# Kernel optimization log

Measured on AMD Instinct MI355X. Metric: run time of the kernel, lower is better.

## Reference

```python
import jax, jax.numpy as jnp
import numpy as np

NUM_TAG = 1024
TAG_DIM = 128
COMMITMENT_COST = 0.25
B, W = 128, 1024


def setup_inputs() -> dict:
    key = jax.random.key(0)
    k1, k2 = jax.random.split(key)
    inputs = jax.random.normal(k1, (B, W, TAG_DIM), dtype=jnp.float32)
    # torch init: uniform_(-1/num_tag, 1/num_tag)
    codebook = jax.random.uniform(k2, (NUM_TAG, TAG_DIM), dtype=jnp.float32,
                                  minval=-1.0 / NUM_TAG, maxval=1.0 / NUM_TAG)
    return {"inputs": inputs, "codebook": codebook}


def reference(inputs, codebook):
    # inputs: [B, W, D], codebook: [K, D]
    D = inputs.shape[-1]
    flat = inputs.reshape(-1, D)  # [N, D]
    distances = (jnp.sum(flat * flat, axis=1, keepdims=True)
                 + jnp.sum(codebook * codebook, axis=1)
                 - 2.0 * flat @ codebook.T)
    encoding_indices = jnp.argmin(distances, axis=1)  # [N]
    quantized = codebook[encoding_indices].reshape(inputs.shape)  # [B, W, D]
    e_latent_loss = jnp.mean((jax.lax.stop_gradient(quantized) - inputs) ** 2)
    q_latent_loss = jnp.mean((quantized - jax.lax.stop_gradient(inputs)) ** 2)
    vq_loss = q_latent_loss + COMMITMENT_COST * e_latent_loss
    # straight-through estimator
    quantized_st = inputs + jax.lax.stop_gradient(quantized - inputs)
    return (quantized_st, vq_loss, encoding_indices.reshape(inputs.shape[:-1]))
```

## Files before the change

kernel.cpp:

```cpp
#include <hip/hip_runtime.h>

#define NUM_TAG 1024
#define TAG_DIM 128
#define NROWS   131072
#define FLAG_M  1.25e-4f
#define RPG     8
#define RF      4

typedef __attribute__((ext_vector_type(8))) short short8;
typedef __attribute__((ext_vector_type(4))) float f32x4;

__device__ inline void split2(float xv, unsigned short& h, unsigned short& m) {
    unsigned xb = __float_as_uint(xv);
    unsigned hb = xb & 0xFFFF0000u;
    float r1 = xv - __uint_as_float(hb);
    unsigned mb = __float_as_uint(r1) & 0xFFFF0000u;
    h = (unsigned short)(hb >> 16);
    m = (unsigned short)(mb >> 16);
}

__device__ inline void gld_lds16(const void* g, void* l) {
    __builtin_amdgcn_global_load_lds(
        (const __attribute__((address_space(1))) void*)g,
        (__attribute__((address_space(3))) void*)l, 16, 0, 0);
}

__global__ __launch_bounds__(256) void prep_kernel(
    const float* __restrict__ cb, float* __restrict__ scc,
    unsigned short* __restrict__ cbf, int* __restrict__ count)
{
    int t = blockIdx.x * 256 + threadIdx.x;
    if (t == 0) count[0] = 0;
    {
        int l  = t & 63;
        int c  = (t >> 6) & 1;
        int s  = (t >> 7) & 3;
        int ch = t >> 9;
        int k  = ch * 32 + c * 16 + (l & 15);
        int d0 = s * 32 + (l >> 4) * 8;
        const float4* xp = reinterpret_cast<const float4*>(cb) + k * 32 + (d0 >> 2);
        float4 v0 = xp[0], v1 = xp[1];
        float xv[8] = {v0.x, v0.y, v0.z, v0.w, v1.x, v1.y, v1.z, v1.w};
        short8 hh, mm;
#pragma unroll
        for (int e = 0; e < 8; ++e) {
            unsigned short h, m;
            split2(xv[e], h, m);
            hh[e] = (short)h; mm[e] = (short)m;
        }
        long baseh = (long)ch * 8192 + (((0 * 8) + s * 2 + c) * 64 + l) * 8;
        long basem = (long)ch * 8192 + (((1 * 8) + s * 2 + c) * 64 + l) * 8;
        *reinterpret_cast<short8*>(cbf + baseh) = hh;
        *reinterpret_cast<short8*>(cbf + basem) = mm;
    }
    if (t < NUM_TAG) {
        const float4* row = reinterpret_cast<const float4*>(cb) + t * (TAG_DIM / 4);
        float s = 0.f;
#pragma unroll
        for (int i = 0; i < TAG_DIM / 4; ++i) {
            float4 v = row[i];
            s += v.x * v.x; s += v.y * v.y; s += v.z * v.z; s += v.w * v.w;
        }
        scc[t] = s;
    }
}

__global__ __launch_bounds__(256, 2) void argmin_mfma_kernel(
    const float* __restrict__ x,
    const unsigned short* __restrict__ cbf,
    const float* __restrict__ scc,
    float* __restrict__ fidx_out,
    int* __restrict__ list, int* __restrict__ count)
{
    __shared__ __align__(16) unsigned short lds[2][8192];
    __shared__ float scc_lds[NUM_TAG];

    const int tid = threadIdx.x;
    const int w   = tid >> 6;
    const int l   = tid & 63;
    const int l15 = l & 15;
    const int l4  = l >> 4;
    const int row0 = blockIdx.x * 256 + w * 64;

    reinterpret_cast<float4*>(scc_lds)[tid] =
        reinterpret_cast<const float4*>(scc)[tid];

    short8 Ah[RF][4], Am[RF][4];
#pragma unroll
    for (int rf = 0; rf < RF; ++rf) {
        const float4* xp = reinterpret_cast<const float4*>(x) +
                           (long)(row0 + rf * 16 + l15) * 32 + l4 * 2;
#pragma unroll
        for (int s = 0; s < 4; ++s) {
            float4 v0 = xp[s * 8];
            float4 v1 = xp[s * 8 + 1];
            float xv[8] = {v0.x, v0.y, v0.z, v0.w, v1.x, v1.y, v1.z, v1.w};
#pragma unroll
            for (int e = 0; e < 8; ++e) {
                unsigned short h, m;
                split2(xv[e], h, m);
                Ah[rf][s][e] = (short)h;
                Am[rf][s][e] = (short)m;
            }
        }
    }

    float m1[RF][4], m2[RF][4]; int i1[RF][4];
#pragma unroll
    for (int rf = 0; rf < RF; ++rf)
#pragma unroll
        for (int r = 0; r < 4; ++r) { m1[rf][r] = 3.4e38f; m2[rf][r] = 3.4e38f; i1[rf][r] = 0; }

    const float4* gsrc = reinterpret_cast<const float4*>(cbf);

#pragma unroll
    for (int i = 0; i < 4; ++i)
        gld_lds16(gsrc + i * 256 + tid, (void*)&lds[0][(i * 256 + tid) * 8]);
    __syncthreads();

    for (int ch = 0; ch < 32; ++ch) {
        const int b = ch & 1;
        if (ch < 31) {
            const float4* gp = gsrc + (ch + 1) * 1024 + tid;
#pragma unroll
            for (int i = 0; i < 4; ++i)
                gld_lds16(gp + i * 256, (void*)&lds[b ^ 1][(i * 256 + tid) * 8]);
        }

        const int col0 = ch << 5;
        f32x4 acc[RF][2];
#pragma unroll
        for (int rf = 0; rf < RF; ++rf)
#pragma unroll
            for (int c = 0; c < 2; ++c) acc[rf][c] = (f32x4)0.f;

#pragma unroll
        for (int s = 0; s < 4; ++s) {
#pragma unroll
            for (int c = 0; c < 2; ++c) {
                const short8 Bh = *reinterpret_cast<const short8*>(
                    &lds[b][(((0 * 8) + s * 2 + c) * 64 + l) * 8]);
                const short8 Bm = *reinterpret_cast<const short8*>(
                    &lds[b][(((1 * 8) + s * 2 + c) * 64 + l) * 8]);
#pragma unroll
                for (int rf = 0; rf < RF; ++rf) {
                    acc[rf][c] = __builtin_amdgcn_mfma_f32_16x16x32_bf16(Ah[rf][s], Bm, acc[rf][c], 0, 0, 0);
                    acc[rf][c] = __builtin_amdgcn_mfma_f32_16x16x32_bf16(Am[rf][s], Bh, acc[rf][c], 0, 0, 0);
                    acc[rf][c] = __builtin_amdgcn_mfma_f32_16x16x32_bf16(Ah[rf][s], Bh, acc[rf][c], 0, 0, 0);
                }
            }
        }

#pragma unroll
        for (int c = 0; c < 2; ++c) {
            const int k = col0 + c * 16 + l15;
            const float sccv = scc_lds[k];
#pragma unroll
            for (int rf = 0; rf < RF; ++rf)
#pragma unroll
                for (int r = 0; r < 4; ++r) {
                    float score = sccv - 2.0f * acc[rf][c][r];
                    m2[rf][r] = __builtin_amdgcn_fmed3f(score, m1[rf][r], m2[rf][r]);
                    i1[rf][r] = (score < m1[rf][r]) ? k : i1[rf][r];
                    m1[rf][r] = fminf(m1[rf][r], score);
                }
        }

        __syncthreads();
    }

#pragma unroll
    for (int rf = 0; rf < RF; ++rf)
#pragma unroll
        for (int r = 0; r < 4; ++r) {
            float v1 = m1[rf][r], v2 = m2[rf][r]; int ii = i1[rf][r];
#pragma unroll
            for (int mk = 1; mk < 16; mk <<= 1) {
                float o1 = __shfl_xor(v1, mk, 64);
                float o2 = __shfl_xor(v2, mk, 64);
                int   oi = __shfl_xor(ii, mk, 64);
                float n2 = fminf(fminf(v2, o2), fmaxf(v1, o1));
                if (o1 < v1 || (o1 == v1 && oi < ii)) { v1 = o1; ii = oi; }
                v2 = n2;
            }
            if (l15 == 0) {
                int row = row0 + rf * 16 + l4 * 4 + r;
                fidx_out[row] = (float)ii;
                if (v2 - v1 <= FLAG_M) {
                    int pos = atomicAdd(count, 1);
                    list[pos] = row;
                }
            }
        }
}

__global__ __launch_bounds__(256) void exact_fix_kernel(
    const float* __restrict__ x, const float* __restrict__ cb,
    const float* __restrict__ scc, const int* __restrict__ list,
    const int* __restrict__ count, float* __restrict__ fidx_out)
{
    __shared__ float4 Xs[RPG][32];
    __shared__ float  sxxs[RPG];
    __shared__ float  wrv[RPG][4];
    __shared__ int    wri[RPG][4];
    __shared__ int    rows_s[RPG];

    const int tid  = threadIdx.x;
    const int lane = tid & 63;
    const int wv   = tid >> 6;
    const int nflag = count[0];
    const int ngroups = (nflag + RPG - 1) / RPG;

    for (int g = blockIdx.x; g < ngroups; g += gridDim.x) {
        const int nr = min(RPG, nflag - g * RPG);
        if (tid < RPG)
            rows_s[tid] = list[g * RPG + min(tid, nr - 1)];
        __syncthreads();
        {
            int r = tid >> 5, i = tid & 31;
            Xs[r][i] = reinterpret_cast<const float4*>(x)[(long)rows_s[r] * 32 + i];
        }
        __syncthreads();
        if (tid < RPG) {
            float s = 0.f;
            for (int i = 0; i < 32; ++i) {
                float4 v = Xs[tid][i];
                s += v.x * v.x; s += v.y * v.y; s += v.z * v.z; s += v.w * v.w;
            }
            sxxs[tid] = s;
        }
        __syncthreads();

        float acc[RPG][4];
#pragma unroll
        for (int r = 0; r < RPG; ++r)
#pragma unroll
            for (int j = 0; j < 4; ++j) acc[r][j] = 0.f;

        const float4* crow = reinterpret_cast<const float4*>(cb) + (tid * 4) * 32;
        for (int i = 0; i < 32; ++i) {
            float4 xv[RPG];
#pragma unroll
            for (int r = 0; r < RPG; ++r) xv[r] = Xs[r][i];
#pragma unroll
            for (int j = 0; j < 4; ++j) {
                float4 c = crow[j * 32 + i];
#pragma unroll
                for (int r = 0; r < RPG; ++r) {
                    acc[r][j] += xv[r].x * c.x;
                    acc[r][j] += xv[r].y * c.y;
                    acc[r][j] += xv[r].z * c.z;
                    acc[r][j] += xv[r].w * c.w;
                }
            }
        }

#pragma unroll
        for (int r = 0; r < RPG; ++r) {
            float bv = 3.4e38f; int bi = 0;
            const float sxxv = sxxs[r];
#pragma unroll
            for (int j = 0; j < 4; ++j) {
                int k = tid * 4 + j;
                float s1 = sxxv + scc[k];
                float dist = s1 - 2.0f * acc[r][j];
                if (dist < bv) { bv = dist; bi = k; }
            }
#pragma unroll
            for (int mk = 1; mk < 64; mk <<= 1) {
                float ov = __shfl_xor(bv, mk, 64);
                int   oi = __shfl_xor(bi, mk, 64);
                if (ov < bv || (ov == bv && oi < bi)) { bv = ov; bi = oi; }
            }
            if (lane == 0) { wrv[r][wv] = bv; wri[r][wv] = bi; }
        }
        __syncthreads();
        if (tid < RPG && tid < nr) {
            float bv = wrv[tid][0]; int bi = wri[tid][0];
#pragma unroll
            for (int e = 1; e < 4; ++e) {
                float v = wrv[tid][e]; int oi = wri[tid][e];
                if (v < bv || (v == bv && oi < bi)) { bv = v; bi = oi; }
            }
            fidx_out[rows_s[tid]] = (float)bi;
        }
        __syncthreads();
    }
}

__global__ __launch_bounds__(256) void quant_kernel(
    const float* __restrict__ x, const float* __restrict__ cb,
    const float* __restrict__ fidx, float* __restrict__ out,
    double* __restrict__ partial)
{
    const int N4 = NROWS * (TAG_DIM / 4);
    double s = 0.0;
    for (int i = blockIdx.x * blockDim.x + threadIdx.x; i < N4; i += gridDim.x * blockDim.x) {
        int n = i >> 5;
        int d4 = i & 31;
        int k = (int)fidx[n];
        float4 xv = reinterpret_cast<const float4*>(x)[i];
        float4 qv = reinterpret_cast<const float4*>(cb)[k * 32 + d4];
        float dx = qv.x - xv.x, dy = qv.y - xv.y, dz = qv.z - xv.z, dw = qv.w - xv.w;
        float4 o;
        o.x = xv.x + dx; o.y = xv.y + dy; o.z = xv.z + dz; o.w = xv.w + dw;
        reinterpret_cast<float4*>(out)[i] = o;
        s += (double)dx * dx; s += (double)dy * dy; s += (double)dz * dz; s += (double)dw * dw;
    }
    __shared__ double sd[256];
    sd[threadIdx.x] = s;
    __syncthreads();
    for (int off = 128; off > 0; off >>= 1) {
        if (threadIdx.x < (unsigned)off) sd[threadIdx.x] += sd[threadIdx.x + off];
        __syncthreads();
    }
    if (threadIdx.x == 0) partial[blockIdx.x] = sd[0];
}

__global__ __launch_bounds__(256) void loss_kernel(
    const double* __restrict__ partial, int n, float* __restrict__ out_loss)
{
    __shared__ double sd[256];
    double s = 0.0;
    for (int i = threadIdx.x; i < n; i += 256) s += partial[i];
    sd[threadIdx.x] = s;
    __syncthreads();
    for (int off = 128; off > 0; off >>= 1) {
        if (threadIdx.x < (unsigned)off) sd[threadIdx.x] += sd[threadIdx.x + off];
        __syncthreads();
    }
    if (threadIdx.x == 0) {
        double mean = sd[0] / (double)((long long)NROWS * TAG_DIM);
        out_loss[0] = (float)(mean + 0.25 * mean);
    }
}

extern "C" void kernel_launch(void* const* d_in, const int* in_sizes, int n_in,
                              void* d_out, int out_size, void* d_ws, size_t ws_size,
                              hipStream_t stream) {
    const float* x  = (const float*)d_in[0];
    const float* cb = (const float*)d_in[1];
    float* out      = (float*)d_out;
    float* out_loss = out + (long)NROWS * TAG_DIM;
    float* out_fidx = out_loss + 1;

    char* wsb = (char*)d_ws;
    float*          scc     = (float*)(wsb);
    unsigned short* cbf     = (unsigned short*)(wsb + 4096);
    int*            list    = (int*)(wsb + 528384);
    int*            count   = (int*)(wsb + 1052672);
    double*         partial = (double*)(wsb + 1052736);

    prep_kernel       <<<64, 256, 0, stream>>>(cb, scc, cbf, count);
    argmin_mfma_kernel<<<NROWS / 256, 256, 0, stream>>>(x, cbf, scc, out_fidx, list, count);
    exact_fix_kernel  <<<512, 256, 0, stream>>>(x, cb, scc, list, count, out_fidx);
    quant_kernel      <<<2048, 256, 0, stream>>>(x, cb, out_fidx, out, partial);
    loss_kernel       <<<1, 256, 0, stream>>>(partial, 2048, out_loss);
}
```

Measured before the change: 245.7 us.

## Load codebook fragments directly from global into registers, dropping LDS staging

Replaces the double-buffered LDS staging of the split-bf16 codebook (global_load_lds plus a barrier per chunk) with per-wave direct global loads into registers. Each chunk's loads are split in two halves and software-pipelined against the MFMA work. The aim is to remove the per-chunk __syncthreads and LDS traffic, relying on L2/L1 caching because every wave reads the same codebook. In exchange it raises register pressure and global load traffic, since each wave now fetches the codebook independently, and global load latency may be exposed.

```diff
diff --git a/kernel.cpp b/kernel.cpp
--- a/kernel.cpp
+++ b/kernel.cpp
@@ -17,12 +17,6 @@
     unsigned mb = __float_as_uint(r1) & 0xFFFF0000u;
     h = (unsigned short)(hb >> 16);
     m = (unsigned short)(mb >> 16);
-}
-
-__device__ inline void gld_lds16(const void* g, void* l) {
-    __builtin_amdgcn_global_load_lds(
-        (const __attribute__((address_space(1))) void*)g,
-        (__attribute__((address_space(3))) void*)l, 16, 0, 0);
 }
 
 __global__ __launch_bounds__(256) void prep_kernel(
@@ -72,7 +66,6 @@
     float* __restrict__ fidx_out,
     int* __restrict__ list, int* __restrict__ count)
 {
-    __shared__ __align__(16) unsigned short lds[2][8192];
     __shared__ float scc_lds[NUM_TAG];
 
     const int tid = threadIdx.x;
@@ -111,46 +104,60 @@
 #pragma unroll
         for (int r = 0; r < 4; ++r) { m1[rf][r] = 3.4e38f; m2[rf][r] = 3.4e38f; i1[rf][r] = 0; }
 
-    const float4* gsrc = reinterpret_cast<const float4*>(cbf);
-
-#pragma unroll
-    for (int i = 0; i < 4; ++i)
-        gld_lds16(gsrc + i * 256 + tid, (void*)&lds[0][(i * 256 + tid) * 8]);
     __syncthreads();
 
+    const unsigned short* gbase = cbf + l * 8;
+
+#define LDB(CH, HH, BH, BM)                                                     \
+    {                                                                           \
+        const unsigned short* p_ = gbase + (CH) * 8192;                         \
+        _Pragma("unroll")                                                       \
+        for (int s2_ = 0; s2_ < 2; ++s2_)                                       \
+            _Pragma("unroll")                                                   \
+            for (int c_ = 0; c_ < 2; ++c_) {                                    \
+                int s_ = (HH) * 2 + s2_;                                        \
+                BH[s2_ * 2 + c_] = *reinterpret_cast<const short8*>(            \
+                    p_ + ((0 * 8 + s_ * 2 + c_) * 64) * 8);                     \
+                BM[s2_ * 2 + c_] = *reinterpret_cast<const short8*>(            \
+                    p_ + ((1 * 8 + s_ * 2 + c_) * 64) * 8);                     \
+            }                                                                   \
+    }
+
+#define CMP(HH, BH, BM)                                                         \
+    {                                                                           \
+        _Pragma("unroll")                                                       \
+        for (int s2_ = 0; s2_ < 2; ++s2_) {                                     \
+            int s_ = (HH) * 2 + s2_;                                            \
+            _Pragma("unroll")                                                   \
+            for (int c_ = 0; c_ < 2; ++c_) {                                    \
+                const short8 Bh_ = BH[s2_ * 2 + c_];                            \
+                const short8 Bm_ = BM[s2_ * 2 + c_];                            \
+                _Pragma("unroll")                                               \
+                for (int rf_ = 0; rf_ < RF; ++rf_) {                            \
+                    acc[rf_][c_] = __builtin_amdgcn_mfma_f32_16x16x32_bf16(Ah[rf_][s_], Bm_, acc[rf_][c_], 0, 0, 0); \
+                    acc[rf_][c_] = __builtin_amdgcn_mfma_f32_16x16x32_bf16(Am[rf_][s_], Bh_, acc[rf_][c_], 0, 0, 0); \
+                    acc[rf_][c_] = __builtin_amdgcn_mfma_f32_16x16x32_bf16(Ah[rf_][s_], Bh_, acc[rf_][c_], 0, 0, 0); \
+                }                                                               \
+            }                                                                   \
+        }                                                                       \
+    }
+
+    short8 BhA[4], BmA[4], BhB[4], BmB[4];
+    LDB(0, 0, BhA, BmA);
+
     for (int ch = 0; ch < 32; ++ch) {
-        const int b = ch & 1;
-        if (ch < 31) {
-            const float4* gp = gsrc + (ch + 1) * 1024 + tid;
-#pragma unroll
-            for (int i = 0; i < 4; ++i)
-                gld_lds16(gp + i * 256, (void*)&lds[b ^ 1][(i * 256 + tid) * 8]);
-        }
+        f32x4 acc[RF][2];
+#pragma unroll
+        for (int rf = 0; rf < RF; ++rf)
+#pragma unroll
+            for (int c = 0; c < 2; ++c) acc[rf][c] = (f32x4)0.f;
+
+        LDB(ch, 1, BhB, BmB);
+        CMP(0, BhA, BmA);
+        if (ch < 31) LDB(ch + 1, 0, BhA, BmA);
+        CMP(1, BhB, BmB);
 
         const int col0 = ch << 5;
-        f32x4 acc[RF][2];
-#pragma unroll
-        for (int rf = 0; rf < RF; ++rf)
-#pragma unroll
-            for (int c = 0; c < 2; ++c) acc[rf][c] = (f32x4)0.f;
-
-#pragma unroll
-        for (int s = 0; s < 4; ++s) {
-#pragma unroll
-            for (int c = 0; c < 2; ++c) {
-                const short8 Bh = *reinterpret_cast<const short8*>(
-                    &lds[b][(((0 * 8) + s * 2 + c) * 64 + l) * 8]);
-                const short8 Bm = *reinterpret_cast<const short8*>(
-                    &lds[b][(((1 * 8) + s * 2 + c) * 64 + l) * 8]);
-#pragma unroll
-                for (int rf = 0; rf < RF; ++rf) {
-                    acc[rf][c] = __builtin_amdgcn_mfma_f32_16x16x32_bf16(Ah[rf][s], Bm, acc[rf][c], 0, 0, 0);
-                    acc[rf][c] = __builtin_amdgcn_mfma_f32_16x16x32_bf16(Am[rf][s], Bh, acc[rf][c], 0, 0, 0);
-                    acc[rf][c] = __builtin_amdgcn_mfma_f32_16x16x32_bf16(Ah[rf][s], Bh, acc[rf][c], 0, 0, 0);
-                }
-            }
-        }
-
 #pragma unroll
         for (int c = 0; c < 2; ++c) {
             const int k = col0 + c * 16 + l15;
@@ -165,9 +172,9 @@
                     m1[rf][r] = fminf(m1[rf][r], score);
                 }
         }
-
-        __syncthreads();
-    }
+    }
+#undef LDB
+#undef CMP
 
 #pragma unroll
     for (int rf = 0; rf < RF; ++rf)
```

After: 260.2 us. +5.9%, slower.

## Use single-wave blocks with per-wave codebook streaming and no block barriers

Applied to the files above, without the earlier changes.

The argmin kernel now runs one 64-thread wavefront per block instead of four waves sharing codebook tiles. Each wave streams 16-code chunks into double-buffered LDS using async global-to-LDS loads issued two chunks ahead, and synchronises with explicit vmcnt/lgkmcnt waits instead of __syncthreads. The prep kernel's codebook layout is changed to match the 16-wide chunks. This removes block-wide barrier stalls, but each wave now loads the whole codebook itself, which multiplies L2/LDS fill traffic by four and adds risk around the hand-placed wait counts.

```diff
diff --git a/kernel.cpp b/kernel.cpp
--- a/kernel.cpp
+++ b/kernel.cpp
@@ -33,10 +33,9 @@
     if (t == 0) count[0] = 0;
     {
         int l  = t & 63;
-        int c  = (t >> 6) & 1;
-        int s  = (t >> 7) & 3;
-        int ch = t >> 9;
-        int k  = ch * 32 + c * 16 + (l & 15);
+        int s  = (t >> 6) & 3;
+        int ch = t >> 8;
+        int k  = ch * 16 + (l & 15);
         int d0 = s * 32 + (l >> 4) * 8;
         const float4* xp = reinterpret_cast<const float4*>(cb) + k * 32 + (d0 >> 2);
         float4 v0 = xp[0], v1 = xp[1];
@@ -48,8 +47,8 @@
             split2(xv[e], h, m);
             hh[e] = (short)h; mm[e] = (short)m;
         }
-        long baseh = (long)ch * 8192 + (((0 * 8) + s * 2 + c) * 64 + l) * 8;
-        long basem = (long)ch * 8192 + (((1 * 8) + s * 2 + c) * 64 + l) * 8;
+        long baseh = (long)ch * 4096 + (((0 * 4) + s) * 64 + l) * 8;
+        long basem = (long)ch * 4096 + (((1 * 4) + s) * 64 + l) * 8;
         *reinterpret_cast<short8*>(cbf + baseh) = hh;
         *reinterpret_cast<short8*>(cbf + basem) = mm;
     }
@@ -65,25 +64,33 @@
     }
 }
 
-__global__ __launch_bounds__(256, 2) void argmin_mfma_kernel(
+__global__ __launch_bounds__(64, 2) void argmin_mfma_kernel(
     const float* __restrict__ x,
     const unsigned short* __restrict__ cbf,
     const float* __restrict__ scc,
     float* __restrict__ fidx_out,
     int* __restrict__ list, int* __restrict__ count)
 {
-    __shared__ __align__(16) unsigned short lds[2][8192];
+    __shared__ __align__(16) unsigned short lds[2][4096];
     __shared__ float scc_lds[NUM_TAG];
 
-    const int tid = threadIdx.x;
-    const int w   = tid >> 6;
-    const int l   = tid & 63;
+    const int l   = threadIdx.x & 63;
     const int l15 = l & 15;
     const int l4  = l >> 4;
-    const int row0 = blockIdx.x * 256 + w * 64;
-
-    reinterpret_cast<float4*>(scc_lds)[tid] =
-        reinterpret_cast<const float4*>(scc)[tid];
+    const int row0 = blockIdx.x * 64;
+
+    const float4* gsrc = reinterpret_cast<const float4*>(cbf);
+
+#pragma unroll
+    for (int i = 0; i < 4; ++i)
+        gld_lds16(reinterpret_cast<const float4*>(scc) + i * 64 + l,
+                  (void*)(scc_lds + (i * 64 + l) * 4));
+#pragma unroll
+    for (int i = 0; i < 8; ++i)
+        gld_lds16(gsrc + i * 64 + l, (void*)&lds[0][(i * 64 + l) * 8]);
+#pragma unroll
+    for (int i = 0; i < 8; ++i)
+        gld_lds16(gsrc + 512 + i * 64 + l, (void*)&lds[1][(i * 64 + l) * 8]);
 
     short8 Ah[RF][4], Am[RF][4];
 #pragma unroll
@@ -111,62 +118,53 @@
 #pragma unroll
         for (int r = 0; r < 4; ++r) { m1[rf][r] = 3.4e38f; m2[rf][r] = 3.4e38f; i1[rf][r] = 0; }
 
-    const float4* gsrc = reinterpret_cast<const float4*>(cbf);
-
-#pragma unroll
-    for (int i = 0; i < 4; ++i)
-        gld_lds16(gsrc + i * 256 + tid, (void*)&lds[0][(i * 256 + tid) * 8]);
-    __syncthreads();
-
-    for (int ch = 0; ch < 32; ++ch) {
+    for (int ch = 0; ch < 64; ++ch) {
         const int b = ch & 1;
-        if (ch < 31) {
-            const float4* gp = gsrc + (ch + 1) * 1024 + tid;
-#pragma unroll
-            for (int i = 0; i < 4; ++i)
-                gld_lds16(gp + i * 256, (void*)&lds[b ^ 1][(i * 256 + tid) * 8]);
-        }
-
-        const int col0 = ch << 5;
-        f32x4 acc[RF][2];
+        if (ch < 63) { asm volatile("s_waitcnt vmcnt(8)" ::: "memory"); }
+        else         { asm volatile("s_waitcnt vmcnt(0)" ::: "memory"); }
+        __builtin_amdgcn_sched_barrier(0);
+
+        short8 Bh[4], Bm[4];
+#pragma unroll
+        for (int s = 0; s < 4; ++s) {
+            Bh[s] = *reinterpret_cast<const short8*>(&lds[b][(((0 * 4) + s) * 64 + l) * 8]);
+            Bm[s] = *reinterpret_cast<const short8*>(&lds[b][(((1 * 4) + s) * 64 + l) * 8]);
+        }
+        const float sccv = scc_lds[ch * 16 + l15];
+
+        asm volatile("s_waitcnt lgkmcnt(0)" ::: "memory");
+        __builtin_amdgcn_sched_barrier(0);
+
+        if (ch + 2 < 64) {
+            const float4* gp = gsrc + (ch + 2) * 512 + l;
+#pragma unroll
+            for (int i = 0; i < 8; ++i)
+                gld_lds16(gp + i * 64, (void*)&lds[b][(i * 64 + l) * 8]);
+        }
+
+        f32x4 acc[RF];
+#pragma unroll
+        for (int rf = 0; rf < RF; ++rf) acc[rf] = (f32x4)0.f;
+
+#pragma unroll
+        for (int s = 0; s < 4; ++s)
+#pragma unroll
+            for (int rf = 0; rf < RF; ++rf) {
+                acc[rf] = __builtin_amdgcn_mfma_f32_16x16x32_bf16(Ah[rf][s], Bm[s], acc[rf], 0, 0, 0);
+                acc[rf] = __builtin_amdgcn_mfma_f32_16x16x32_bf16(Am[rf][s], Bh[s], acc[rf], 0, 0, 0);
+                acc[rf] = __builtin_amdgcn_mfma_f32_16x16x32_bf16(Ah[rf][s], Bh[s], acc[rf], 0, 0, 0);
+            }
+
+        const int k = ch * 16 + l15;
 #pragma unroll
         for (int rf = 0; rf < RF; ++rf)
 #pragma unroll
-            for (int c = 0; c < 2; ++c) acc[rf][c] = (f32x4)0.f;
-
-#pragma unroll
-        for (int s = 0; s < 4; ++s) {
-#pragma unroll
-            for (int c = 0; c < 2; ++c) {
-                const short8 Bh = *reinterpret_cast<const short8*>(
-                    &lds[b][(((0 * 8) + s * 2 + c) * 64 + l) * 8]);
-                const short8 Bm = *reinterpret_cast<const short8*>(
-                    &lds[b][(((1 * 8) + s * 2 + c) * 64 + l) * 8]);
-#pragma unroll
-                for (int rf = 0; rf < RF; ++rf) {
-                    acc[rf][c] = __builtin_amdgcn_mfma_f32_16x16x32_bf16(Ah[rf][s], Bm, acc[rf][c], 0, 0, 0);
-                    acc[rf][c] = __builtin_amdgcn_mfma_f32_16x16x32_bf16(Am[rf][s], Bh, acc[rf][c], 0, 0, 0);
-                    acc[rf][c] = __builtin_amdgcn_mfma_f32_16x16x32_bf16(Ah[rf][s], Bh, acc[rf][c], 0, 0, 0);
-                }
-            }
-        }
-
-#pragma unroll
-        for (int c = 0; c < 2; ++c) {
-            const int k = col0 + c * 16 + l15;
-            const float sccv = scc_lds[k];
-#pragma unroll
-            for (int rf = 0; rf < RF; ++rf)
-#pragma unroll
-                for (int r = 0; r < 4; ++r) {
-                    float score = sccv - 2.0f * acc[rf][c][r];
-                    m2[rf][r] = __builtin_amdgcn_fmed3f(score, m1[rf][r], m2[rf][r]);
-                    i1[rf][r] = (score < m1[rf][r]) ? k : i1[rf][r];
-                    m1[rf][r] = fminf(m1[rf][r], score);
-                }
-        }
-
-        __syncthreads();
+            for (int r = 0; r < 4; ++r) {
+                float score = sccv - 2.0f * acc[rf][r];
+                m2[rf][r] = __builtin_amdgcn_fmed3f(score, m1[rf][r], m2[rf][r]);
+                i1[rf][r] = (score < m1[rf][r]) ? k : i1[rf][r];
+                m1[rf][r] = fminf(m1[rf][r], score);
+            }
     }
 
 #pragma unroll
@@ -352,7 +350,7 @@
     double*         partial = (double*)(wsb + 1052736);
 
     prep_kernel       <<<64, 256, 0, stream>>>(cb, scc, cbf, count);
-    argmin_mfma_kernel<<<NROWS / 256, 256, 0, stream>>>(x, cbf, scc, out_fidx, list, count);
+    argmin_mfma_kernel<<<NROWS / 64, 64, 0, stream>>>(x, cbf, scc, out_fidx, list, count);
     exact_fix_kernel  <<<512, 256, 0, stream>>>(x, cb, scc, list, count, out_fidx);
     quant_kernel      <<<2048, 256, 0, stream>>>(x, cb, out_fidx, out, partial);
     loss_kernel       <<<1, 256, 0, stream>>>(partial, 2048, out_loss);
```

New measurement: 249.1 us. No clear change (+1.4%).
